# Optimization experiments

Hardware: AMD Instinct MI355X
Metric: run time of the kernel (lower is better)

Reference implementation:

```python
import jax, jax.numpy as jnp
import numpy as np

DIM, K_NN, RADIUS, HIDDEN = 128, 4, 2.5, 64
B, T, N = 32, 64, 25


def setup_inputs() -> dict:
    key = jax.random.key(0)
    ks = jax.random.split(key, 12)
    s = 0.02
    return {
        "emb": jax.random.normal(ks[0], (B, T, N, DIM), jnp.float32),
        "bboxes": jax.random.uniform(ks[1], (B, T, N, 4), jnp.float32),
        "person_mask": jax.random.uniform(ks[2], (B, T, N)) < 0.9,
        "edge_w1": jax.random.normal(ks[3], (2 * DIM + 3, HIDDEN), jnp.float32) * s,
        "edge_b1": jnp.zeros((HIDDEN,), jnp.float32),
        "edge_w2": jax.random.normal(ks[4], (HIDDEN, DIM), jnp.float32) * s,
        "edge_b2": jnp.zeros((DIM,), jnp.float32),
        "node_w1": jax.random.normal(ks[5], (2 * DIM, HIDDEN), jnp.float32) * s,
        "node_b1": jnp.zeros((HIDDEN,), jnp.float32),
        "node_w2": jax.random.normal(ks[6], (HIDDEN, DIM), jnp.float32) * s,
        "node_b2": jnp.zeros((DIM,), jnp.float32),
        "ln_g": jnp.ones((DIM,), jnp.float32),
        "ln_b": jnp.zeros((DIM,), jnp.float32),
    }


def _forward(emb, bboxes, person_mask, edge_w1, edge_b1, edge_w2, edge_b2,
             node_w1, node_b1, node_w2, node_b2, ln_g, ln_b):
    b, t, n, d = emb.shape
    BT = b * t
    x = emb.reshape(BT, n, d)
    boxes = bboxes.reshape(BT, n, 4)
    mask = person_mask.reshape(BT, n)

    cx, cy = boxes[..., 0], boxes[..., 1]
    h = jnp.maximum(boxes[..., 3], 1e-6)
    dx = cx[:, :, None] - cx[:, None, :]            # [BT,N,N]
    dy = cy[:, :, None] - cy[:, None, :]
    dist = jnp.sqrt(dx * dx + dy * dy + 1e-6)
    scale = h[:, :, None]
    dx_n, dy_n, dist_n = dx / scale, dy / scale, dist / scale

    eye = jnp.eye(n, dtype=bool)[None]
    pair_valid = (mask[:, :, None] & mask[:, None, :]) & ~eye
    dist_for_knn = jnp.where(pair_valid, dist_n, 1e6)

    K = min(K_NN, max(n - 1, 1))
    neg_d, knn_idx = jax.lax.top_k(-dist_for_knn, K)  # smallest-K -> [BT,N,K]
    knn_dist = -neg_d

    nbr_valid = jnp.take_along_axis(pair_valid, knn_idx, axis=2)
    nbr_valid = nbr_valid & (knn_dist < RADIUS)

    # gather neighbor features: [BT,N,K,D]
    bt_idx = jnp.arange(BT)[:, None, None]
    x_j = x[bt_idx, knn_idx]
    x_i = jnp.broadcast_to(x[:, :, None, :], (BT, n, K, d))
    edge_all = jnp.stack([dx_n, dy_n, dist_n], axis=-1)  # [BT,N,N,3]
    e_ij = jnp.take_along_axis(edge_all, knn_idx[..., None], axis=2)  # [BT,N,K,3]

    msg_in = jnp.concatenate([x_i, x_j, e_ij], axis=-1)  # [BT,N,K,2D+3]
    msg = jax.nn.relu(msg_in @ edge_w1 + edge_b1) @ edge_w2 + edge_b2
    nbr_f = nbr_valid.astype(msg.dtype)
    msg = msg * nbr_f[..., None]
    denom = jnp.maximum(nbr_f.sum(axis=2, keepdims=True), 1.0)
    agg = msg.sum(axis=2) / denom                    # [BT,N,D]

    upd_in = jnp.concatenate([x, agg], axis=-1)
    delta = jax.nn.relu(upd_in @ node_w1 + node_b1) @ node_w2 + node_b2
    has_nbr = jnp.any(nbr_valid, axis=2, keepdims=True)
    delta = delta * has_nbr.astype(delta.dtype)

    y = x + delta
    mu = y.mean(axis=-1, keepdims=True)
    var = y.var(axis=-1, keepdims=True)
    y = (y - mu) * jax.lax.rsqrt(var + 1e-5) * ln_g + ln_b
    out = y * mask[..., None].astype(y.dtype)
    return out.reshape(b, t, n, d)


def reference(emb, bboxes, person_mask, edge_w1, edge_b1, edge_w2, edge_b2,
              node_w1, node_b1, node_w2, node_b2, ln_g, ln_b):
    return _forward(emb, bboxes, person_mask, edge_w1, edge_b1, edge_w2, edge_b2,
                    node_w1, node_b1, node_w2, node_b2, ln_g, ln_b)
```

## Files before the change

kernel.cpp:

```cpp
#include <hip/hip_runtime.h>

#define NN   25
#define DD   128
#define HH   64
#define KK   4
#define RADF 2.5f

#define XBP  136
#define HSP  72
#define AGP  136

#define O_W1T 0
#define O_W2T 16896
#define O_N1T 25088
#define O_N2T 41472

typedef __attribute__((ext_vector_type(8))) short  short8;
typedef __attribute__((ext_vector_type(4))) float  f32x4;

__device__ __forceinline__ ushort f2bf(float x) {
    uint u = __float_as_uint(x);
    u += 0x7fffu + ((u >> 16) & 1u);
    return (ushort)(u >> 16);
}
__device__ __forceinline__ float bf2f(ushort u) {
    return __uint_as_float((uint)u << 16);
}
__device__ __forceinline__ uint pack2(float a, float b) {
    return (uint)f2bf(a) | ((uint)f2bf(b) << 16);
}
__device__ __forceinline__ short8 ldw(const ushort* p) {
    return *reinterpret_cast<const short8*>(p);
}
#define MFMA16(a, b, c) __builtin_amdgcn_mfma_f32_16x16x32_bf16((a), (b), (c), 0, 0, 0)

__global__ void prep_kernel(const float* __restrict__ ew1, const float* __restrict__ ew2,
                            const float* __restrict__ nw1, const float* __restrict__ nw2,
                            ushort* __restrict__ w) {
    int tid = blockIdx.x * blockDim.x + threadIdx.x;
    int stride = gridDim.x * blockDim.x;
    for (int e = tid; e < 259 * 64; e += stride) {
        int k = e >> 6, c = e & 63;
        w[O_W1T + c * 264 + k] = f2bf(ew1[e]);
    }
    for (int e = tid; e < 64 * 128; e += stride) {
        int k = e >> 7, d = e & 127;
        w[O_W2T + d * 64 + k] = f2bf(ew2[e]);
    }
    for (int e = tid; e < 256 * 64; e += stride) {
        int k = e >> 6, c = e & 63;
        w[O_N1T + c * 256 + k] = f2bf(nw1[e]);
    }
    for (int e = tid; e < 64 * 128; e += stride) {
        int k = e >> 7, d = e & 127;
        w[O_N2T + d * 64 + k] = f2bf(nw2[e]);
    }
}

__global__ __launch_bounds__(128, 4) void ig10_kernel(
    const float* __restrict__ emb,
    const float* __restrict__ bboxes,
    const int*   __restrict__ pmask,
    const float* __restrict__ ew1f,
    const float* __restrict__ eb1,
    const float* __restrict__ eb2,
    const float* __restrict__ nb1,
    const float* __restrict__ nb2,
    const float* __restrict__ lng,
    const float* __restrict__ lnb,
    const ushort* __restrict__ W,
    float* __restrict__ out)
{
    const int bt  = blockIdx.x;
    const int t   = threadIdx.x;
    const int wv  = t >> 6;
    const int ln  = t & 63;
    const int g   = ln >> 4;
    const int r16 = ln & 15;
    const int cb  = 2 * wv;
    const int cb4 = 4 * wv;

    __shared__ ushort s_xb[NN * XBP];
    __shared__ __align__(16) char s_R[7200];
    __shared__ ushort s_g1v[NN * HSP];
    __shared__ __align__(16) char s_misc[1600];
    __shared__ short  s_idxs[NN][KK];
    __shared__ float  s_meta[NN][4];

    float (*s_ev)[KK][4] = reinterpret_cast<float(*)[KK][4]>(s_misc);
    float (*s_red)[2][2] = reinterpret_cast<float(*)[2][2]>(s_misc);
    ushort* s_hxi = reinterpret_cast<ushort*>(s_R);
    ushort* s_hs  = reinterpret_cast<ushort*>(s_R + 3600);
    ushort* s_ag  = reinterpret_cast<ushort*>(s_R);

    if (wv == 0) {
        const float4* src4 = reinterpret_cast<const float4*>(emb + (size_t)bt * (NN * DD));
        for (int u = ln; u < NN * 16; u += 64) {
            int row = u >> 4, q = u & 15;
            float4 f0 = src4[row * 32 + q * 2];
            float4 f1 = src4[row * 32 + q * 2 + 1];
            uint4 p;
            p.x = pack2(f0.x, f0.y); p.y = pack2(f0.z, f0.w);
            p.z = pack2(f1.x, f1.y); p.w = pack2(f1.z, f1.w);
            *reinterpret_cast<uint4*>(&s_xb[row * XBP + q * 8]) = p;
        }
    } else {
        const int n = (ln < NN) ? ln : NN - 1;
        const float4 b4 = *reinterpret_cast<const float4*>(bboxes + ((size_t)bt * NN + n) * 4);
        const float cxn = b4.x, cyn = b4.y;
        const float hvn = fmaxf(b4.w, 1e-6f);
        const int   mn  = pmask[(size_t)bt * NN + n];
        const float inv = 1.0f / hvn;
        float best[KK] = {1e30f, 1e30f, 1e30f, 1e30f};
        int   bidx[KK] = {0, 0, 0, 0};
        for (int j = 0; j < NN; ++j) {
            float cxj = __shfl(cxn, j);
            float cyj = __shfl(cyn, j);
            int   mj  = __shfl(mn, j);
            float dx = cxn - cxj, dy = cyn - cyj;
            float dn = sqrtf(fmaf(dx, dx, fmaf(dy, dy, 1e-6f))) * inv;
            bool  pv = (mn != 0) && (mj != 0) && (j != n);
            float cv = pv ? dn : 1e6f;
            int   ci = j;
#pragma unroll
            for (int kk = 0; kk < KK; ++kk) {
                if (cv < best[kk]) {
                    float tv = best[kk]; best[kk] = cv; cv = tv;
                    int   ti = bidx[kk]; bidx[kk] = ci; ci = ti;
                }
            }
        }
        float cnt = 0.f;
        float e0v[KK], e1v[KK], e2v[KK], vvv[KK];
#pragma unroll
        for (int k = 0; k < KK; ++k) {
            int bj = bidx[k];
            float cxb = __shfl(cxn, bj);
            float cyb = __shfl(cyn, bj);
            float val = (best[k] < RADF) ? 1.f : 0.f;
            cnt += val;
            float dx = cxn - cxb, dy = cyn - cyb;
            e0v[k] = dx * inv;
            e1v[k] = dy * inv;
            e2v[k] = sqrtf(fmaf(dx, dx, fmaf(dy, dy, 1e-6f))) * inv;
            vvv[k] = val;
        }
        if (ln < NN) {
#pragma unroll
            for (int k = 0; k < KK; ++k) {
                s_ev[n][k][0] = e0v[k];
                s_ev[n][k][1] = e1v[k];
                s_ev[n][k][2] = e2v[k];
                s_ev[n][k][3] = vvv[k];
                s_idxs[n][k]  = (short)bidx[k];
            }
            s_meta[n][0] = cnt;
            s_meta[n][1] = 1.0f / fmaxf(cnt, 1.0f);
            s_meta[n][2] = (cnt > 0.f) ? 1.f : 0.f;
            s_meta[n][3] = mn ? 1.f : 0.f;
        }
    }
    __syncthreads();

    {
        int na1 = 16 + r16; if (na1 > 24) na1 = 24;
        const ushort* A0 = s_xb + r16 * XBP + g * 8;
        const ushort* A1 = s_xb + na1 * XBP + g * 8;
        f32x4 c[2][2] = {};
#pragma unroll
        for (int kt = 0; kt < 4; ++kt) {
            short8 b0 = ldw(W + O_W1T + (size_t)(16 * (cb + 0) + r16) * 264 + kt * 32 + g * 8);
            short8 b1 = ldw(W + O_W1T + (size_t)(16 * (cb + 1) + r16) * 264 + kt * 32 + g * 8);
            short8 a0 = ldw(A0 + kt * 32);
            short8 a1 = ldw(A1 + kt * 32);
            c[0][0] = MFMA16(a0, b0, c[0][0]); c[0][1] = MFMA16(a0, b1, c[0][1]);
            c[1][0] = MFMA16(a1, b0, c[1][0]); c[1][1] = MFMA16(a1, b1, c[1][1]);
        }
#pragma unroll
        for (int mt = 0; mt < 2; ++mt)
#pragma unroll
            for (int q = 0; q < 4; ++q) {
                int nr = 16 * mt + 4 * g + q;
                if (nr < 25) {
#pragma unroll
                    for (int ntl = 0; ntl < 2; ++ntl)
                        s_hxi[nr * HSP + 16 * (cb + ntl) + r16] = f2bf(c[mt][ntl][q]);
                }
            }
    }

    {
        int jn[7];
#pragma unroll
        for (int T = 0; T < 7; ++T) {
            int r = 16 * T + r16; if (r > 99) r = 99;
            jn[T] = s_idxs[r >> 2][r & 3];
        }
        f32x4 c[7][2] = {};
#pragma unroll
        for (int kt = 0; kt < 4; ++kt) {
            short8 b0 = ldw(W + O_W1T + (size_t)(16 * (cb + 0) + r16) * 264 + 128 + kt * 32 + g * 8);
            short8 b1 = ldw(W + O_W1T + (size_t)(16 * (cb + 1) + r16) * 264 + 128 + kt * 32 + g * 8);
#pragma unroll
            for (int T = 0; T < 7; ++T) {
                short8 a = ldw(s_xb + jn[T] * XBP + kt * 32 + g * 8);
                c[T][0] = MFMA16(a, b0, c[T][0]);
                c[T][1] = MFMA16(a, b1, c[T][1]);
            }
        }
        float we0[2], we1[2], we2[2], bb1[2];
#pragma unroll
        for (int ntl = 0; ntl < 2; ++ntl) {
            int col = 16 * (cb + ntl) + r16;
            we0[ntl] = ew1f[256 * 64 + col];
            we1[ntl] = ew1f[257 * 64 + col];
            we2[ntl] = ew1f[258 * 64 + col];
            bb1[ntl] = eb1[col];
        }
#pragma unroll
        for (int T = 0; T < 7; ++T) {
            const int n = 4 * T + g;
            if (n < 25) {
                float v0 = s_ev[n][0][3], v1 = s_ev[n][1][3];
                float v2 = s_ev[n][2][3], v3 = s_ev[n][3][3];
                float e0q[4], e1q[4], e2q[4];
#pragma unroll
                for (int q = 0; q < 4; ++q) {
                    e0q[q] = s_ev[n][q][0]; e1q[q] = s_ev[n][q][1]; e2q[q] = s_ev[n][q][2];
                }
#pragma unroll
                for (int ntl = 0; ntl < 2; ++ntl) {
                    int col = 16 * (cb + ntl) + r16;
                    float base = bb1[ntl] + bf2f(s_hxi[n * HSP + col]);
                    float p0 = c[T][ntl][0] + base + e0q[0] * we0[ntl] + e1q[0] * we1[ntl] + e2q[0] * we2[ntl];
                    float p1 = c[T][ntl][1] + base + e0q[1] * we0[ntl] + e1q[1] * we1[ntl] + e2q[1] * we2[ntl];
                    float p2 = c[T][ntl][2] + base + e0q[2] * we0[ntl] + e1q[2] * we1[ntl] + e2q[2] * we2[ntl];
                    float p3 = c[T][ntl][3] + base + e0q[3] * we0[ntl] + e1q[3] * we1[ntl] + e2q[3] * we2[ntl];
                    float hs = fmaf(v0, fmaxf(p0, 0.f),
                               fmaf(v1, fmaxf(p1, 0.f),
                               fmaf(v2, fmaxf(p2, 0.f),
                                    v3 * fmaxf(p3, 0.f))));
                    s_hs[n * HSP + col] = f2bf(hs);
                }
            }
        }
    }
    __syncthreads();

    {
        int na1 = 16 + r16; if (na1 > 24) na1 = 24;
        const ushort* A0 = s_hs + r16 * HSP + g * 8;
        const ushort* A1 = s_hs + na1 * HSP + g * 8;
        f32x4 c[2][4] = {};
#pragma unroll
        for (int kt = 0; kt < 2; ++kt) {
            short8 a0 = ldw(A0 + kt * 32);
            short8 a1 = ldw(A1 + kt * 32);
#pragma unroll
            for (int ntl = 0; ntl < 4; ++ntl) {
                short8 b = ldw(W + O_W2T + (size_t)(16 * (cb4 + ntl) + r16) * 64 + kt * 32 + g * 8);
                c[0][ntl] = MFMA16(a0, b, c[0][ntl]);
                c[1][ntl] = MFMA16(a1, b, c[1][ntl]);
            }
        }
        __syncthreads();
#pragma unroll
        for (int ntl = 0; ntl < 4; ++ntl) {
            int col = 16 * (cb4 + ntl) + r16;
            float b2c = eb2[col];
#pragma unroll
            for (int mt = 0; mt < 2; ++mt)
#pragma unroll
                for (int q = 0; q < 4; ++q) {
                    int nr = 16 * mt + 4 * g + q;
                    if (nr < 25) {
                        float agv = s_meta[nr][1] * fmaf(s_meta[nr][0], b2c, c[mt][ntl][q]);
                        s_ag[nr * AGP + col] = f2bf(agv);
                    }
                }
        }
    }
    __syncthreads();

    {
        int na1 = 16 + r16; if (na1 > 24) na1 = 24;
        const ushort* Ax0 = s_xb + r16 * XBP + g * 8;
        const ushort* Ax1 = s_xb + na1 * XBP + g * 8;
        const ushort* Aa0 = s_ag + r16 * AGP + g * 8;
        const ushort* Aa1 = s_ag + na1 * AGP + g * 8;
        f32x4 c[2][2] = {};
#pragma unroll
        for (int kt = 0; kt < 8; ++kt) {
            const ushort* Ap0 = (kt < 4) ? (Ax0 + kt * 32) : (Aa0 + (kt - 4) * 32);
            const ushort* Ap1 = (kt < 4) ? (Ax1 + kt * 32) : (Aa1 + (kt - 4) * 32);
            short8 a0 = ldw(Ap0);
            short8 a1 = ldw(Ap1);
#pragma unroll
            for (int ntl = 0; ntl < 2; ++ntl) {
                short8 b = ldw(W + O_N1T + (size_t)(16 * (cb + ntl) + r16) * 256 + kt * 32 + g * 8);
                c[0][ntl] = MFMA16(a0, b, c[0][ntl]);
                c[1][ntl] = MFMA16(a1, b, c[1][ntl]);
            }
        }
#pragma unroll
        for (int ntl = 0; ntl < 2; ++ntl) {
            int col = 16 * (cb + ntl) + r16;
            float b1c = nb1[col];
#pragma unroll
            for (int mt = 0; mt < 2; ++mt)
#pragma unroll
                for (int q = 0; q < 4; ++q) {
                    int nr = 16 * mt + 4 * g + q;
                    if (nr < 25)
                        s_g1v[nr * HSP + col] = f2bf(fmaxf(c[mt][ntl][q] + b1c, 0.f));
                }
        }
    }
    __syncthreads();

    {
        int na1 = 16 + r16; if (na1 > 24) na1 = 24;
        const ushort* A0 = s_g1v + r16 * HSP + g * 8;
        const ushort* A1 = s_g1v + na1 * HSP + g * 8;
        f32x4 c[2][4] = {};
#pragma unroll
        for (int kt = 0; kt < 2; ++kt) {
            short8 a0 = ldw(A0 + kt * 32);
            short8 a1 = ldw(A1 + kt * 32);
#pragma unroll
            for (int ntl = 0; ntl < 4; ++ntl) {
                short8 b = ldw(W + O_N2T + (size_t)(16 * (cb4 + ntl) + r16) * 64 + kt * 32 + g * 8);
                c[0][ntl] = MFMA16(a0, b, c[0][ntl]);
                c[1][ntl] = MFMA16(a1, b, c[1][ntl]);
            }
        }
        float nb2c[4], glc[4], blc[4];
#pragma unroll
        for (int ntl = 0; ntl < 4; ++ntl) {
            int col = 16 * (cb4 + ntl) + r16;
            nb2c[ntl] = nb2[col];
            glc[ntl]  = lng[col];
            blc[ntl]  = lnb[col];
        }
        float y[2][4][4];
#pragma unroll
        for (int mt = 0; mt < 2; ++mt) {
#pragma unroll
            for (int q = 0; q < 4; ++q) {
                int nr = 16 * mt + 4 * g + q;
                int nc = nr < 25 ? nr : 24;
                float has = s_meta[nc][2];
                float a = 0.f, b = 0.f;
#pragma unroll
                for (int ntl = 0; ntl < 4; ++ntl) {
                    int col = 16 * (cb4 + ntl) + r16;
                    float yv = fmaf(has, c[mt][ntl][q] + nb2c[ntl], bf2f(s_xb[nc * XBP + col]));
                    y[mt][ntl][q] = yv;
                    a += yv;
                    b = fmaf(yv, yv, b);
                }
#pragma unroll
                for (int o = 1; o < 16; o <<= 1) {
                    a += __shfl_xor(a, o);
                    b += __shfl_xor(b, o);
                }
                if (r16 == 0 && nr < 25) {
                    s_red[nr][wv][0] = a;
                    s_red[nr][wv][1] = b;
                }
            }
        }
        __syncthreads();
#pragma unroll
        for (int mt = 0; mt < 2; ++mt) {
#pragma unroll
            for (int q = 0; q < 4; ++q) {
                int nr = 16 * mt + 4 * g + q;
                int nc = nr < 25 ? nr : 24;
                float S   = s_red[nc][0][0] + s_red[nc][1][0];
                float S2  = s_red[nc][0][1] + s_red[nc][1][1];
                float mu  = S * (1.0f / 128.0f);
                float var = S2 * (1.0f / 128.0f) - mu * mu;
                float rs  = rsqrtf(var + 1e-5f);
                float mk  = s_meta[nc][3];
                if (nr < 25) {
                    float* op = out + (size_t)bt * (NN * DD) + nr * DD;
#pragma unroll
                    for (int ntl = 0; ntl < 4; ++ntl) {
                        int col = 16 * (cb4 + ntl) + r16;
                        op[col] = fmaf((y[mt][ntl][q] - mu) * rs, glc[ntl], blc[ntl]) * mk;
                    }
                }
            }
        }
    }
}

extern "C" void kernel_launch(void* const* d_in, const int* in_sizes, int n_in,
                              void* d_out, int out_size, void* d_ws, size_t ws_size,
                              hipStream_t stream) {
    const float* emb    = (const float*)d_in[0];
    const float* bboxes = (const float*)d_in[1];
    const int*   pmask  = (const int*)  d_in[2];
    const float* ew1    = (const float*)d_in[3];
    const float* eb1    = (const float*)d_in[4];
    const float* ew2    = (const float*)d_in[5];
    const float* eb2    = (const float*)d_in[6];
    const float* nw1    = (const float*)d_in[7];
    const float* nb1    = (const float*)d_in[8];
    const float* nw2    = (const float*)d_in[9];
    const float* nb2    = (const float*)d_in[10];
    const float* lng    = (const float*)d_in[11];
    const float* lnb    = (const float*)d_in[12];
    float* out = (float*)d_out;
    ushort* W  = (ushort*)d_ws;

    prep_kernel<<<64, 256, 0, stream>>>(ew1, ew2, nw1, nw2, W);

    const int BT = in_sizes[2] / NN;
    ig10_kernel<<<BT, 128, 0, stream>>>(
        emb, bboxes, pmask, ew1, eb1, eb2, nb1, nb2, lng, lnb, W, out);
}
```

Before: 42.63 us.

## Split per-block work across four waves instead of two

```diff
diff --git a/kernel.cpp b/kernel.cpp
--- a/kernel.cpp
+++ b/kernel.cpp
@@ -57,7 +57,7 @@
     }
 }
 
-__global__ __launch_bounds__(128, 4) void ig10_kernel(
+__global__ __launch_bounds__(256, 8) void ig11_kernel(
     const float* __restrict__ emb,
     const float* __restrict__ bboxes,
     const int*   __restrict__ pmask,
@@ -77,8 +77,7 @@
     const int ln  = t & 63;
     const int g   = ln >> 4;
     const int r16 = ln & 15;
-    const int cb  = 2 * wv;
-    const int cb4 = 4 * wv;
+    const int cb2 = 2 * wv;
 
     __shared__ ushort s_xb[NN * XBP];
     __shared__ __align__(16) char s_R[7200];
@@ -88,14 +87,15 @@
     __shared__ float  s_meta[NN][4];
 
     float (*s_ev)[KK][4] = reinterpret_cast<float(*)[KK][4]>(s_misc);
-    float (*s_red)[2][2] = reinterpret_cast<float(*)[2][2]>(s_misc);
+    float (*s_red)[4][2] = reinterpret_cast<float(*)[4][2]>(s_misc);
     ushort* s_hxi = reinterpret_cast<ushort*>(s_R);
     ushort* s_hs  = reinterpret_cast<ushort*>(s_R + 3600);
     ushort* s_ag  = reinterpret_cast<ushort*>(s_R);
 
-    if (wv == 0) {
+    if (wv != 1) {
         const float4* src4 = reinterpret_cast<const float4*>(emb + (size_t)bt * (NN * DD));
-        for (int u = ln; u < NN * 16; u += 64) {
+        const int wid = (wv == 0) ? 0 : (wv - 1);
+        for (int u = wid * 64 + ln; u < NN * 16; u += 192) {
             int row = u >> 4, q = u & 15;
             float4 f0 = src4[row * 32 + q * 2];
             float4 f1 = src4[row * 32 + q * 2 + 1];
@@ -166,27 +166,23 @@
         int na1 = 16 + r16; if (na1 > 24) na1 = 24;
         const ushort* A0 = s_xb + r16 * XBP + g * 8;
         const ushort* A1 = s_xb + na1 * XBP + g * 8;
-        f32x4 c[2][2] = {};
+        f32x4 c0 = {0,0,0,0}, c1 = {0,0,0,0};
 #pragma unroll
         for (int kt = 0; kt < 4; ++kt) {
-            short8 b0 = ldw(W + O_W1T + (size_t)(16 * (cb + 0) + r16) * 264 + kt * 32 + g * 8);
-            short8 b1 = ldw(W + O_W1T + (size_t)(16 * (cb + 1) + r16) * 264 + kt * 32 + g * 8);
+            short8 b  = ldw(W + O_W1T + (size_t)(16 * wv + r16) * 264 + kt * 32 + g * 8);
             short8 a0 = ldw(A0 + kt * 32);
             short8 a1 = ldw(A1 + kt * 32);
-            c[0][0] = MFMA16(a0, b0, c[0][0]); c[0][1] = MFMA16(a0, b1, c[0][1]);
-            c[1][0] = MFMA16(a1, b0, c[1][0]); c[1][1] = MFMA16(a1, b1, c[1][1]);
-        }
-#pragma unroll
-        for (int mt = 0; mt < 2; ++mt)
-#pragma unroll
-            for (int q = 0; q < 4; ++q) {
-                int nr = 16 * mt + 4 * g + q;
-                if (nr < 25) {
-#pragma unroll
-                    for (int ntl = 0; ntl < 2; ++ntl)
-                        s_hxi[nr * HSP + 16 * (cb + ntl) + r16] = f2bf(c[mt][ntl][q]);
-                }
-            }
+            c0 = MFMA16(a0, b, c0);
+            c1 = MFMA16(a1, b, c1);
+        }
+        const int col = 16 * wv + r16;
+#pragma unroll
+        for (int q = 0; q < 4; ++q) {
+            int nr0 = 4 * g + q;
+            int nr1 = 16 + 4 * g + q;
+            s_hxi[nr0 * HSP + col] = f2bf(c0[q]);
+            if (nr1 < 25) s_hxi[nr1 * HSP + col] = f2bf(c1[q]);
+        }
     }
 
     {
@@ -196,52 +192,37 @@
             int r = 16 * T + r16; if (r > 99) r = 99;
             jn[T] = s_idxs[r >> 2][r & 3];
         }
-        f32x4 c[7][2] = {};
+        f32x4 c[7] = {};
 #pragma unroll
         for (int kt = 0; kt < 4; ++kt) {
-            short8 b0 = ldw(W + O_W1T + (size_t)(16 * (cb + 0) + r16) * 264 + 128 + kt * 32 + g * 8);
-            short8 b1 = ldw(W + O_W1T + (size_t)(16 * (cb + 1) + r16) * 264 + 128 + kt * 32 + g * 8);
+            short8 b = ldw(W + O_W1T + (size_t)(16 * wv + r16) * 264 + 128 + kt * 32 + g * 8);
 #pragma unroll
             for (int T = 0; T < 7; ++T) {
                 short8 a = ldw(s_xb + jn[T] * XBP + kt * 32 + g * 8);
-                c[T][0] = MFMA16(a, b0, c[T][0]);
-                c[T][1] = MFMA16(a, b1, c[T][1]);
-            }
-        }
-        float we0[2], we1[2], we2[2], bb1[2];
-#pragma unroll
-        for (int ntl = 0; ntl < 2; ++ntl) {
-            int col = 16 * (cb + ntl) + r16;
-            we0[ntl] = ew1f[256 * 64 + col];
-            we1[ntl] = ew1f[257 * 64 + col];
-            we2[ntl] = ew1f[258 * 64 + col];
-            bb1[ntl] = eb1[col];
-        }
+                c[T] = MFMA16(a, b, c[T]);
+            }
+        }
+        const int col = 16 * wv + r16;
+        const float we0 = ew1f[256 * 64 + col];
+        const float we1 = ew1f[257 * 64 + col];
+        const float we2 = ew1f[258 * 64 + col];
+        const float bb1 = eb1[col];
 #pragma unroll
         for (int T = 0; T < 7; ++T) {
             const int n = 4 * T + g;
             if (n < 25) {
                 float v0 = s_ev[n][0][3], v1 = s_ev[n][1][3];
                 float v2 = s_ev[n][2][3], v3 = s_ev[n][3][3];
-                float e0q[4], e1q[4], e2q[4];
-#pragma unroll
-                for (int q = 0; q < 4; ++q) {
-                    e0q[q] = s_ev[n][q][0]; e1q[q] = s_ev[n][q][1]; e2q[q] = s_ev[n][q][2];
-                }
-#pragma unroll
-                for (int ntl = 0; ntl < 2; ++ntl) {
-                    int col = 16 * (cb + ntl) + r16;
-                    float base = bb1[ntl] + bf2f(s_hxi[n * HSP + col]);
-                    float p0 = c[T][ntl][0] + base + e0q[0] * we0[ntl] + e1q[0] * we1[ntl] + e2q[0] * we2[ntl];
-                    float p1 = c[T][ntl][1] + base + e0q[1] * we0[ntl] + e1q[1] * we1[ntl] + e2q[1] * we2[ntl];
-                    float p2 = c[T][ntl][2] + base + e0q[2] * we0[ntl] + e1q[2] * we1[ntl] + e2q[2] * we2[ntl];
-                    float p3 = c[T][ntl][3] + base + e0q[3] * we0[ntl] + e1q[3] * we1[ntl] + e2q[3] * we2[ntl];
-                    float hs = fmaf(v0, fmaxf(p0, 0.f),
-                               fmaf(v1, fmaxf(p1, 0.f),
-                               fmaf(v2, fmaxf(p2, 0.f),
-                                    v3 * fmaxf(p3, 0.f))));
-                    s_hs[n * HSP + col] = f2bf(hs);
-                }
+                float base = bb1 + bf2f(s_hxi[n * HSP + col]);
+                float p0 = c[T][0] + base + s_ev[n][0][0] * we0 + s_ev[n][0][1] * we1 + s_ev[n][0][2] * we2;
+                float p1 = c[T][1] + base + s_ev[n][1][0] * we0 + s_ev[n][1][1] * we1 + s_ev[n][1][2] * we2;
+                float p2 = c[T][2] + base + s_ev[n][2][0] * we0 + s_ev[n][2][1] * we1 + s_ev[n][2][2] * we2;
+                float p3 = c[T][3] + base + s_ev[n][3][0] * we0 + s_ev[n][3][1] * we1 + s_ev[n][3][2] * we2;
+                float hs = fmaf(v0, fmaxf(p0, 0.f),
+                           fmaf(v1, fmaxf(p1, 0.f),
+                           fmaf(v2, fmaxf(p2, 0.f),
+                                v3 * fmaxf(p3, 0.f))));
+                s_hs[n * HSP + col] = f2bf(hs);
             }
         }
     }
@@ -251,22 +232,22 @@
         int na1 = 16 + r16; if (na1 > 24) na1 = 24;
         const ushort* A0 = s_hs + r16 * HSP + g * 8;
         const ushort* A1 = s_hs + na1 * HSP + g * 8;
-        f32x4 c[2][4] = {};
+        f32x4 c[2][2] = {};
 #pragma unroll
         for (int kt = 0; kt < 2; ++kt) {
             short8 a0 = ldw(A0 + kt * 32);
             short8 a1 = ldw(A1 + kt * 32);
 #pragma unroll
-            for (int ntl = 0; ntl < 4; ++ntl) {
-                short8 b = ldw(W + O_W2T + (size_t)(16 * (cb4 + ntl) + r16) * 64 + kt * 32 + g * 8);
+            for (int ntl = 0; ntl < 2; ++ntl) {
+                short8 b = ldw(W + O_W2T + (size_t)(16 * (cb2 + ntl) + r16) * 64 + kt * 32 + g * 8);
                 c[0][ntl] = MFMA16(a0, b, c[0][ntl]);
                 c[1][ntl] = MFMA16(a1, b, c[1][ntl]);
             }
         }
         __syncthreads();
 #pragma unroll
-        for (int ntl = 0; ntl < 4; ++ntl) {
-            int col = 16 * (cb4 + ntl) + r16;
+        for (int ntl = 0; ntl < 2; ++ntl) {
+            int col = 16 * (cb2 + ntl) + r16;
             float b2c = eb2[col];
 #pragma unroll
             for (int mt = 0; mt < 2; ++mt)
@@ -288,32 +269,25 @@
         const ushort* Ax1 = s_xb + na1 * XBP + g * 8;
         const ushort* Aa0 = s_ag + r16 * AGP + g * 8;
         const ushort* Aa1 = s_ag + na1 * AGP + g * 8;
-        f32x4 c[2][2] = {};
+        f32x4 c0 = {0,0,0,0}, c1 = {0,0,0,0};
 #pragma unroll
         for (int kt = 0; kt < 8; ++kt) {
             const ushort* Ap0 = (kt < 4) ? (Ax0 + kt * 32) : (Aa0 + (kt - 4) * 32);
             const ushort* Ap1 = (kt < 4) ? (Ax1 + kt * 32) : (Aa1 + (kt - 4) * 32);
             short8 a0 = ldw(Ap0);
             short8 a1 = ldw(Ap1);
-#pragma unroll
-            for (int ntl = 0; ntl < 2; ++ntl) {
-                short8 b = ldw(W + O_N1T + (size_t)(16 * (cb + ntl) + r16) * 256 + kt * 32 + g * 8);
-                c[0][ntl] = MFMA16(a0, b, c[0][ntl]);
-                c[1][ntl] = MFMA16(a1, b, c[1][ntl]);
-            }
-        }
-#pragma unroll
-        for (int ntl = 0; ntl < 2; ++ntl) {
-            int col = 16 * (cb + ntl) + r16;
-            float b1c = nb1[col];
-#pragma unroll
-            for (int mt = 0; mt < 2; ++mt)
-#pragma unroll
-                for (int q = 0; q < 4; ++q) {
-                    int nr = 16 * mt + 4 * g + q;
-                    if (nr < 25)
-                        s_g1v[nr * HSP + col] = f2bf(fmaxf(c[mt][ntl][q] + b1c, 0.f));
-                }
+            short8 b  = ldw(W + O_N1T + (size_t)(16 * wv + r16) * 256 + kt * 32 + g * 8);
+            c0 = MFMA16(a0, b, c0);
+            c1 = MFMA16(a1, b, c1);
+        }
+        const int col = 16 * wv + r16;
+        const float b1c = nb1[col];
+#pragma unroll
+        for (int q = 0; q < 4; ++q) {
+            int nr0 = 4 * g + q;
+            int nr1 = 16 + 4 * g + q;
+            s_g1v[nr0 * HSP + col] = f2bf(fmaxf(c0[q] + b1c, 0.f));
+            if (nr1 < 25) s_g1v[nr1 * HSP + col] = f2bf(fmaxf(c1[q] + b1c, 0.f));
         }
     }
     __syncthreads();
@@ -322,27 +296,27 @@
         int na1 = 16 + r16; if (na1 > 24) na1 = 24;
         const ushort* A0 = s_g1v + r16 * HSP + g * 8;
         const ushort* A1 = s_g1v + na1 * HSP + g * 8;
-        f32x4 c[2][4] = {};
+        f32x4 c[2][2] = {};
 #pragma unroll
         for (int kt = 0; kt < 2; ++kt) {
             short8 a0 = ldw(A0 + kt * 32);
             short8 a1 = ldw(A1 + kt * 32);
 #pragma unroll
-            for (int ntl = 0; ntl < 4; ++ntl) {
-                short8 b = ldw(W + O_N2T + (size_t)(16 * (cb4 + ntl) + r16) * 64 + kt * 32 + g * 8);
+            for (int ntl = 0; ntl < 2; ++ntl) {
+                short8 b = ldw(W + O_N2T + (size_t)(16 * (cb2 + ntl) + r16) * 64 + kt * 32 + g * 8);
                 c[0][ntl] = MFMA16(a0, b, c[0][ntl]);
                 c[1][ntl] = MFMA16(a1, b, c[1][ntl]);
             }
         }
-        float nb2c[4], glc[4], blc[4];
-#pragma unroll
-        for (int ntl = 0; ntl < 4; ++ntl) {
-            int col = 16 * (cb4 + ntl) + r16;
+        float nb2c[2], glc[2], blc[2];
+#pragma unroll
+        for (int ntl = 0; ntl < 2; ++ntl) {
+            int col = 16 * (cb2 + ntl) + r16;
             nb2c[ntl] = nb2[col];
             glc[ntl]  = lng[col];
             blc[ntl]  = lnb[col];
         }
-        float y[2][4][4];
+        float y[2][2][4];
 #pragma unroll
         for (int mt = 0; mt < 2; ++mt) {
 #pragma unroll
@@ -352,8 +326,8 @@
                 float has = s_meta[nc][2];
                 float a = 0.f, b = 0.f;
 #pragma unroll
-                for (int ntl = 0; ntl < 4; ++ntl) {
-                    int col = 16 * (cb4 + ntl) + r16;
+                for (int ntl = 0; ntl < 2; ++ntl) {
+                    int col = 16 * (cb2 + ntl) + r16;
                     float yv = fmaf(has, c[mt][ntl][q] + nb2c[ntl], bf2f(s_xb[nc * XBP + col]));
                     y[mt][ntl][q] = yv;
                     a += yv;
@@ -377,8 +351,8 @@
             for (int q = 0; q < 4; ++q) {
                 int nr = 16 * mt + 4 * g + q;
                 int nc = nr < 25 ? nr : 24;
-                float S   = s_red[nc][0][0] + s_red[nc][1][0];
-                float S2  = s_red[nc][0][1] + s_red[nc][1][1];
+                float S   = (s_red[nc][0][0] + s_red[nc][1][0]) + (s_red[nc][2][0] + s_red[nc][3][0]);
+                float S2  = (s_red[nc][0][1] + s_red[nc][1][1]) + (s_red[nc][2][1] + s_red[nc][3][1]);
                 float mu  = S * (1.0f / 128.0f);
                 float var = S2 * (1.0f / 128.0f) - mu * mu;
                 float rs  = rsqrtf(var + 1e-5f);
@@ -386,8 +360,8 @@
                 if (nr < 25) {
                     float* op = out + (size_t)bt * (NN * DD) + nr * DD;
 #pragma unroll
-                    for (int ntl = 0; ntl < 4; ++ntl) {
-                        int col = 16 * (cb4 + ntl) + r16;
+                    for (int ntl = 0; ntl < 2; ++ntl) {
+                        int col = 16 * (cb2 + ntl) + r16;
                         op[col] = fmaf((y[mt][ntl][q] - mu) * rs, glc[ntl], blc[ntl]) * mk;
                     }
                 }
@@ -418,6 +392,6 @@
     prep_kernel<<<64, 256, 0, stream>>>(ew1, ew2, nw1, nw2, W);
 
     const int BT = in_sizes[2] / NN;
-    ig10_kernel<<<BT, 128, 0, stream>>>(
+    ig11_kernel<<<BT, 256, 0, stream>>>(
         emb, bboxes, pmask, ew1, eb1, eb2, nb1, nb2, lng, lnb, W, out);
 }
```

New measurement: 46.64 us. 1.09x slower.

## Fold edge second layer into node first layer via precomputed weight product

Applied to the files above, without the earlier changes.

```diff
diff --git a/kernel.cpp b/kernel.cpp
--- a/kernel.cpp
+++ b/kernel.cpp
@@ -8,12 +8,12 @@
 
 #define XBP  136
 #define HSP  72
-#define AGP  136
-
-#define O_W1T 0
-#define O_W2T 16896
-#define O_N1T 25088
-#define O_N2T 41472
+
+#define O_W1T  0
+#define O_W2NT 16896
+#define O_N1LO 20992
+#define O_N2T  29184
+#define O_B2N  37376
 
 typedef __attribute__((ext_vector_type(8))) short  short8;
 typedef __attribute__((ext_vector_type(4))) float  f32x4;
@@ -35,8 +35,8 @@
 #define MFMA16(a, b, c) __builtin_amdgcn_mfma_f32_16x16x32_bf16((a), (b), (c), 0, 0, 0)
 
 __global__ void prep_kernel(const float* __restrict__ ew1, const float* __restrict__ ew2,
-                            const float* __restrict__ nw1, const float* __restrict__ nw2,
-                            ushort* __restrict__ w) {
+                            const float* __restrict__ eb2, const float* __restrict__ nw1,
+                            const float* __restrict__ nw2, ushort* __restrict__ w) {
     int tid = blockIdx.x * blockDim.x + threadIdx.x;
     int stride = gridDim.x * blockDim.x;
     for (int e = tid; e < 259 * 64; e += stride) {
@@ -44,26 +44,34 @@
         w[O_W1T + c * 264 + k] = f2bf(ew1[e]);
     }
     for (int e = tid; e < 64 * 128; e += stride) {
-        int k = e >> 7, d = e & 127;
-        w[O_W2T + d * 64 + k] = f2bf(ew2[e]);
-    }
-    for (int e = tid; e < 256 * 64; e += stride) {
-        int k = e >> 6, c = e & 63;
-        w[O_N1T + c * 256 + k] = f2bf(nw1[e]);
-    }
-    for (int e = tid; e < 64 * 128; e += stride) {
-        int k = e >> 7, d = e & 127;
-        w[O_N2T + d * 64 + k] = f2bf(nw2[e]);
-    }
-}
-
-__global__ __launch_bounds__(128, 4) void ig10_kernel(
+        int c = e >> 7, k = e & 127;
+        w[O_N1LO + e] = f2bf(nw1[(size_t)k * 64 + c]);
+    }
+    for (int e = tid; e < 128 * 64; e += stride) {
+        int d = e >> 6, k = e & 63;
+        w[O_N2T + e] = f2bf(nw2[(size_t)k * 128 + d]);
+    }
+    for (int e = tid; e < 64 * 64; e += stride) {
+        int c = e >> 6, k = e & 63;
+        float acc = 0.f;
+        for (int d = 0; d < DD; ++d)
+            acc += ew2[(size_t)k * DD + d] * nw1[(size_t)(DD + d) * HH + c];
+        w[O_W2NT + e] = f2bf(acc);
+    }
+    for (int c = tid; c < HH; c += stride) {
+        float acc = 0.f;
+        for (int d = 0; d < DD; ++d)
+            acc += eb2[d] * nw1[(size_t)(DD + d) * HH + c];
+        reinterpret_cast<float*>(w + O_B2N)[c] = acc;
+    }
+}
+
+__global__ __launch_bounds__(128, 4) void ig12_kernel(
     const float* __restrict__ emb,
     const float* __restrict__ bboxes,
     const int*   __restrict__ pmask,
     const float* __restrict__ ew1f,
     const float* __restrict__ eb1,
-    const float* __restrict__ eb2,
     const float* __restrict__ nb1,
     const float* __restrict__ nb2,
     const float* __restrict__ lng,
@@ -81,17 +89,16 @@
     const int cb4 = 4 * wv;
 
     __shared__ ushort s_xb[NN * XBP];
-    __shared__ __align__(16) char s_R[7200];
-    __shared__ ushort s_g1v[NN * HSP];
+    __shared__ ushort s_hxi[NN * HSP];
+    __shared__ ushort s_hs[NN * HSP];
+    __shared__ ushort s_nxi[NN * HSP];
     __shared__ __align__(16) char s_misc[1600];
     __shared__ short  s_idxs[NN][KK];
     __shared__ float  s_meta[NN][4];
 
     float (*s_ev)[KK][4] = reinterpret_cast<float(*)[KK][4]>(s_misc);
     float (*s_red)[2][2] = reinterpret_cast<float(*)[2][2]>(s_misc);
-    ushort* s_hxi = reinterpret_cast<ushort*>(s_R);
-    ushort* s_hs  = reinterpret_cast<ushort*>(s_R + 3600);
-    ushort* s_ag  = reinterpret_cast<ushort*>(s_R);
+    ushort* s_g1v = s_hxi;
 
     if (wv == 0) {
         const float4* src4 = reinterpret_cast<const float4*>(emb + (size_t)bt * (NN * DD));
@@ -166,15 +173,21 @@
         int na1 = 16 + r16; if (na1 > 24) na1 = 24;
         const ushort* A0 = s_xb + r16 * XBP + g * 8;
         const ushort* A1 = s_xb + na1 * XBP + g * 8;
-        f32x4 c[2][2] = {};
+        f32x4 ce[2][2] = {};
+        f32x4 cn[2][2] = {};
 #pragma unroll
         for (int kt = 0; kt < 4; ++kt) {
-            short8 b0 = ldw(W + O_W1T + (size_t)(16 * (cb + 0) + r16) * 264 + kt * 32 + g * 8);
-            short8 b1 = ldw(W + O_W1T + (size_t)(16 * (cb + 1) + r16) * 264 + kt * 32 + g * 8);
             short8 a0 = ldw(A0 + kt * 32);
             short8 a1 = ldw(A1 + kt * 32);
-            c[0][0] = MFMA16(a0, b0, c[0][0]); c[0][1] = MFMA16(a0, b1, c[0][1]);
-            c[1][0] = MFMA16(a1, b0, c[1][0]); c[1][1] = MFMA16(a1, b1, c[1][1]);
+#pragma unroll
+            for (int ntl = 0; ntl < 2; ++ntl) {
+                short8 be = ldw(W + O_W1T  + (size_t)(16 * (cb + ntl) + r16) * 264 + kt * 32 + g * 8);
+                short8 bn = ldw(W + O_N1LO + (size_t)(16 * (cb + ntl) + r16) * 128 + kt * 32 + g * 8);
+                ce[0][ntl] = MFMA16(a0, be, ce[0][ntl]);
+                ce[1][ntl] = MFMA16(a1, be, ce[1][ntl]);
+                cn[0][ntl] = MFMA16(a0, bn, cn[0][ntl]);
+                cn[1][ntl] = MFMA16(a1, bn, cn[1][ntl]);
+            }
         }
 #pragma unroll
         for (int mt = 0; mt < 2; ++mt)
@@ -183,8 +196,11 @@
                 int nr = 16 * mt + 4 * g + q;
                 if (nr < 25) {
 #pragma unroll
-                    for (int ntl = 0; ntl < 2; ++ntl)
-                        s_hxi[nr * HSP + 16 * (cb + ntl) + r16] = f2bf(c[mt][ntl][q]);
+                    for (int ntl = 0; ntl < 2; ++ntl) {
+                        int col = 16 * (cb + ntl) + r16;
+                        s_hxi[nr * HSP + col] = f2bf(ce[mt][ntl][q]);
+                        s_nxi[nr * HSP + col] = f2bf(cn[mt][ntl][q]);
+                    }
                 }
             }
     }
@@ -251,68 +267,34 @@
         int na1 = 16 + r16; if (na1 > 24) na1 = 24;
         const ushort* A0 = s_hs + r16 * HSP + g * 8;
         const ushort* A1 = s_hs + na1 * HSP + g * 8;
-        f32x4 c[2][4] = {};
+        f32x4 c[2][2] = {};
 #pragma unroll
         for (int kt = 0; kt < 2; ++kt) {
             short8 a0 = ldw(A0 + kt * 32);
             short8 a1 = ldw(A1 + kt * 32);
 #pragma unroll
-            for (int ntl = 0; ntl < 4; ++ntl) {
-                short8 b = ldw(W + O_W2T + (size_t)(16 * (cb4 + ntl) + r16) * 64 + kt * 32 + g * 8);
+            for (int ntl = 0; ntl < 2; ++ntl) {
+                short8 b = ldw(W + O_W2NT + (size_t)(16 * (cb + ntl) + r16) * 64 + kt * 32 + g * 8);
                 c[0][ntl] = MFMA16(a0, b, c[0][ntl]);
                 c[1][ntl] = MFMA16(a1, b, c[1][ntl]);
             }
         }
-        __syncthreads();
-#pragma unroll
-        for (int ntl = 0; ntl < 4; ++ntl) {
-            int col = 16 * (cb4 + ntl) + r16;
-            float b2c = eb2[col];
+        const float* b2Np = reinterpret_cast<const float*>(W + O_B2N);
+#pragma unroll
+        for (int ntl = 0; ntl < 2; ++ntl) {
+            int col = 16 * (cb + ntl) + r16;
+            float b2n = b2Np[col];
+            float b1c = nb1[col];
 #pragma unroll
             for (int mt = 0; mt < 2; ++mt)
 #pragma unroll
                 for (int q = 0; q < 4; ++q) {
                     int nr = 16 * mt + 4 * g + q;
                     if (nr < 25) {
-                        float agv = s_meta[nr][1] * fmaf(s_meta[nr][0], b2c, c[mt][ntl][q]);
-                        s_ag[nr * AGP + col] = f2bf(agv);
+                        float v = bf2f(s_nxi[nr * HSP + col]) + b1c
+                                + s_meta[nr][1] * fmaf(s_meta[nr][0], b2n, c[mt][ntl][q]);
+                        s_g1v[nr * HSP + col] = f2bf(fmaxf(v, 0.f));
                     }
-                }
-        }
-    }
-    __syncthreads();
-
-    {
-        int na1 = 16 + r16; if (na1 > 24) na1 = 24;
-        const ushort* Ax0 = s_xb + r16 * XBP + g * 8;
-        const ushort* Ax1 = s_xb + na1 * XBP + g * 8;
-        const ushort* Aa0 = s_ag + r16 * AGP + g * 8;
-        const ushort* Aa1 = s_ag + na1 * AGP + g * 8;
-        f32x4 c[2][2] = {};
-#pragma unroll
-        for (int kt = 0; kt < 8; ++kt) {
-            const ushort* Ap0 = (kt < 4) ? (Ax0 + kt * 32) : (Aa0 + (kt - 4) * 32);
-            const ushort* Ap1 = (kt < 4) ? (Ax1 + kt * 32) : (Aa1 + (kt - 4) * 32);
-            short8 a0 = ldw(Ap0);
-            short8 a1 = ldw(Ap1);
-#pragma unroll
-            for (int ntl = 0; ntl < 2; ++ntl) {
-                short8 b = ldw(W + O_N1T + (size_t)(16 * (cb + ntl) + r16) * 256 + kt * 32 + g * 8);
-                c[0][ntl] = MFMA16(a0, b, c[0][ntl]);
-                c[1][ntl] = MFMA16(a1, b, c[1][ntl]);
-            }
-        }
-#pragma unroll
-        for (int ntl = 0; ntl < 2; ++ntl) {
-            int col = 16 * (cb + ntl) + r16;
-            float b1c = nb1[col];
-#pragma unroll
-            for (int mt = 0; mt < 2; ++mt)
-#pragma unroll
-                for (int q = 0; q < 4; ++q) {
-                    int nr = 16 * mt + 4 * g + q;
-                    if (nr < 25)
-                        s_g1v[nr * HSP + col] = f2bf(fmaxf(c[mt][ntl][q] + b1c, 0.f));
                 }
         }
     }
@@ -415,9 +397,9 @@
     float* out = (float*)d_out;
     ushort* W  = (ushort*)d_ws;
 
-    prep_kernel<<<64, 256, 0, stream>>>(ew1, ew2, nw1, nw2, W);
+    prep_kernel<<<64, 256, 0, stream>>>(ew1, ew2, eb2, nw1, nw2, W);
 
     const int BT = in_sizes[2] / NN;
-    ig10_kernel<<<BT, 128, 0, stream>>>(
-        emb, bboxes, pmask, ew1, eb1, eb2, nb1, nb2, lng, lnb, W, out);
-}
+    ig12_kernel<<<BT, 128, 0, stream>>>(
+        emb, bboxes, pmask, ew1, eb1, nb1, nb2, lng, lnb, W, out);
+}
```

Result: no change. 42.73 us (+0.2%).
